# Kernel tuning notes

Measured on AMD Instinct MI355X. Metric: run time of the kernel, lower is better.

## Reference

```python
import jax, jax.numpy as jnp
import numpy as np

B, T, H = 128, 500, 512  # batch, time steps, hidden size; wx has 2H features


def setup_inputs() -> dict:
    key = jax.random.key(0)
    k1, k2, k3, k4 = jax.random.split(key, 4)
    wx = jax.random.normal(k1, (B, T, 2 * H), dtype=jnp.float32)
    u = jax.random.normal(k2, (2 * H, H), dtype=jnp.float32) * 0.05  # recurrent weight
    ht = jax.random.normal(k3, (B, H), dtype=jnp.float32)
    drop_mask = jax.random.uniform(k4, (B, H), dtype=jnp.float32)
    return {"wx": wx, "u": u, "ht": ht, "drop_mask": drop_mask}


def reference(wx, u, ht, drop_mask):
    """LiGRU cell forward: sequential recurrence over time via lax.scan.

    wx: [B, T, 2H] linearly transformed input
    u:  [2H, H]    recurrent weight
    ht: [B, H]     initial hidden state
    drop_mask: [B, H] dropout mask applied to candidate at every step
    Returns (ht, zt, at, hcand) each [B, T, H].
    """
    uT = u.T  # [H, 2H]

    def step(h, wx_t):
        gates = wx_t + h @ uT              # [B, 2H]
        at, zt_pre = jnp.split(gates, 2, axis=1)
        zt = jax.nn.sigmoid(zt_pre)
        hcand = jax.nn.relu(at) * drop_mask  # act='relu'
        h_new = h * zt + (1.0 - zt) * hcand
        return h_new, (h_new, zt, at, hcand)

    wx_t_major = jnp.swapaxes(wx, 0, 1)     # [T, B, 2H]
    _, (hs, zs, ats, hcs) = jax.lax.scan(step, ht, wx_t_major)
    tr = lambda x: jnp.swapaxes(x, 0, 1)    # [T,B,H] -> [B,T,H]
    return tr(hs), tr(zs), tr(ats), tr(hcs)
```

## Files before the change

### kernel.cpp

```cpp
#include <hip/hip_runtime.h>
#include <hip/hip_fp16.h>

#define BB 128
#define TT 500
#define HH 512
#define TWOH 1024
#define KB 16

typedef _Float16 f16x8 __attribute__((ext_vector_type(8)));
typedef float f32x4 __attribute__((ext_vector_type(4)));
typedef unsigned long long u64;

#define WS_U16_HALVES (TWOH * HH)
#define HX_WORDS (8 * 2 * 16 * HH)

__global__ void prep_kernel(const float* __restrict__ u,
                            const float* __restrict__ ht,
                            __half* __restrict__ u16,
                            unsigned* __restrict__ hx) {
  int i = blockIdx.x * blockDim.x + threadIdx.x;
  if (i < WS_U16_HALVES) u16[i] = __float2half(u[i]);
  if (i < HX_WORDS) {
    int g = i >> 14, rem = i & 16383;
    int par = rem >> 13, m = (rem >> 9) & 15, k = rem & 511;
    unsigned val;
    if (par == 0) {
      int R = g * 16 + m;
      val = (unsigned)__half_as_ushort(__float2half(ht[(size_t)R * HH + k]));
    } else {
      val = 0xFFFF0000u;
    }
    hx[i] = val;
  }
}

#define TAGMASK 0xFFFF0000FFFF0000ull

__global__ __launch_bounds__(256, 1) void ligru_mfma(
    const float* __restrict__ wx, const __half* __restrict__ u16,
    const float* __restrict__ ht, const float* __restrict__ mask,
    float* __restrict__ out, unsigned* __restrict__ hx) {
  const int tid = threadIdx.x;
  const int lane = tid & 63;
  const int w = tid >> 6;
  const int l15 = lane & 15;
  const int q = lane >> 4;
  const int b = blockIdx.x;
  const int g = b >> 3;
  const int s = b & 7;
  const int row0 = g * 16;
  const int j = s * 64 + w * 16 + l15;

  const bool own = (tid >= s * 32) && (tid < s * 32 + 32);

  __shared__ alignas(16) char hsm[2][16 * 1024];

  f16x8 bf[KB][2];
#pragma unroll
  for (int kb = 0; kb < KB; ++kb) {
    bf[kb][0] = *(const f16x8*)(u16 + (size_t)j * HH + kb * 32 + q * 8);
    bf[kb][1] = *(const f16x8*)(u16 + (size_t)(HH + j) * HH + kb * 32 + q * 8);
  }

  float hreg[4], mreg[4];
#pragma unroll
  for (int r = 0; r < 4; ++r) {
    size_t off = (size_t)(row0 + 4 * q + r) * HH + j;
    mreg[r] = mask[off];
    hreg[r] = ht[off];
  }

  const size_t BTH = (size_t)BB * TT * HH;
  float* out_h = out;
  float* out_z = out + BTH;
  float* out_a = out + 2 * BTH;
  float* out_hc = out + 3 * BTH;

  const u64* hxg = (const u64*)hx + ((size_t)g << 13);

  u64 qw[16];
#pragma unroll
  for (int pp = 0; pp < 16; ++pp)
    qw[pp] = __hip_atomic_load(hxg + pp * 256 + tid, __ATOMIC_RELAXED,
                               __HIP_MEMORY_SCOPE_AGENT);

  float wxa[4], wxz[4], wxa_n[4], wxz_n[4];
#pragma unroll
  for (int r = 0; r < 4; ++r) {
    size_t base = (size_t)(row0 + 4 * q + r) * TT * TWOH + j;
    wxa[r] = wx[base];
    wxz[r] = wx[base + HH];
  }

  for (int t = 0; t < TT; ++t) {
    const int par = t & 1;

    {
      const int tn = (t + 1 < TT) ? t + 1 : t;
#pragma unroll
      for (int r = 0; r < 4; ++r) {
        size_t base = ((size_t)(row0 + 4 * q + r) * TT + tn) * TWOH + j;
        wxa_n[r] = wx[base];
        wxz_n[r] = wx[base + HH];
      }
    }

    {
      const bool skip = own && (t > 0);
      const u64* src = hxg + par * 4096 + tid;
      const u64 tagp = ((u64)(unsigned)t << 48) | ((u64)(unsigned)t << 16);
      bool ok = true;
#pragma unroll
      for (int pp = 0; pp < 16; ++pp) ok &= ((qw[pp] & TAGMASK) == tagp);
      ok |= skip;
      if (!__all(ok)) {
        if (!skip) {
#pragma unroll
          for (int pp = 0; pp < 16; ++pp)
            qw[pp] = __hip_atomic_load(src + pp * 256, __ATOMIC_RELAXED,
                                       __HIP_MEMORY_SCOPE_AGENT);
          ok = true;
#pragma unroll
          for (int pp = 0; pp < 16; ++pp) ok &= ((qw[pp] & TAGMASK) == tagp);
        }
        int bail = 0;
        while (!__all(ok)) {
          __builtin_amdgcn_s_sleep(1);
          if (!skip) {
#pragma unroll
            for (int pp = 0; pp < 16; ++pp)
              qw[pp] = __hip_atomic_load(src + pp * 256, __ATOMIC_RELAXED,
                                         __HIP_MEMORY_SCOPE_AGENT);
            ok = true;
#pragma unroll
            for (int pp = 0; pp < 16; ++pp) ok &= ((qw[pp] & TAGMASK) == tagp);
          }
          if (++bail > (1 << 15)) break;
        }
      }
    }

    if (!(own && t > 0)) {
      char* dst = hsm[par];
#pragma unroll
      for (int pp = 0; pp < 16; ++pp) {
        unsigned d0 = (unsigned)qw[pp], d1 = (unsigned)(qw[pp] >> 32);
        unsigned pk = (d0 & 0xFFFFu) | (d1 << 16);
        *(unsigned*)(dst + ((pp * 1024 + tid * 4) ^ ((pp & 7) << 4))) = pk;
      }
    }
    __syncthreads();

    f32x4 acc0 = {0.f, 0.f, 0.f, 0.f}, acc1 = {0.f, 0.f, 0.f, 0.f};
#pragma unroll
    for (int kb = 0; kb < KB; ++kb) {
      int off = (l15 * 1024 + kb * 64 + q * 16) ^ ((l15 & 7) << 4);
      f16x8 af = *(const f16x8*)(hsm[par] + off);
      acc0 = __builtin_amdgcn_mfma_f32_16x16x32_f16(af, bf[kb][0], acc0, 0, 0, 0);
      acc1 = __builtin_amdgcn_mfma_f32_16x16x32_f16(af, bf[kb][1], acc1, 0, 0, 0);
    }

    unsigned* hd = hx + ((size_t)(g * 2 + (par ^ 1)) << 13);
    const unsigned tg = (unsigned)(t + 1) << 16;
    char* ldst = hsm[par ^ 1];
    float atv[4], ztv[4], hcv[4];
    __half hh[4];
#pragma unroll
    for (int r = 0; r < 4; ++r) {
      float at = acc0[r] + wxa[r];
      float zp = acc1[r] + wxz[r];
      float zt = 1.f / (1.f + __expf(-zp));
      float hc = fmaxf(at, 0.f) * mreg[r];
      float hn = hreg[r] * zt + (1.f - zt) * hc;
      hreg[r] = hn;
      hh[r] = __float2half(hn);
      __hip_atomic_store(hd + (4 * q + r) * HH + j,
                         tg | (unsigned)__half_as_ushort(hh[r]),
                         __ATOMIC_RELAXED, __HIP_MEMORY_SCOPE_AGENT);
      atv[r] = at;
      ztv[r] = zt;
      hcv[r] = hc;
    }

#pragma unroll
    for (int r = 0; r < 4; ++r) {
      const int m = 4 * q + r;
      *(__half*)(ldst + ((m * 1024 + j * 2) ^ ((m & 7) << 4))) = hh[r];
    }

    if (t + 1 < TT && !own) {
      const u64* srcn = hxg + (par ^ 1) * 4096 + tid;
#pragma unroll
      for (int pp = 0; pp < 16; ++pp)
        qw[pp] = __hip_atomic_load(srcn + pp * 256, __ATOMIC_RELAXED,
                                   __HIP_MEMORY_SCOPE_AGENT);
    }

#pragma unroll
    for (int r = 0; r < 4; ++r) {
      size_t oi = ((size_t)(row0 + 4 * q + r) * TT + t) * HH + j;
      __builtin_nontemporal_store(hreg[r], &out_h[oi]);
      __builtin_nontemporal_store(ztv[r], &out_z[oi]);
      __builtin_nontemporal_store(atv[r], &out_a[oi]);
      __builtin_nontemporal_store(hcv[r], &out_hc[oi]);
    }

#pragma unroll
    for (int r = 0; r < 4; ++r) {
      wxa[r] = wxa_n[r];
      wxz[r] = wxz_n[r];
    }
  }
}

extern "C" void kernel_launch(void* const* d_in, const int* in_sizes, int n_in,
                              void* d_out, int out_size, void* d_ws,
                              size_t ws_size, hipStream_t stream) {
  const float* wx = (const float*)d_in[0];
  const float* u = (const float*)d_in[1];
  const float* ht = (const float*)d_in[2];
  const float* mask = (const float*)d_in[3];
  float* out = (float*)d_out;

  __half* u16 = (__half*)d_ws;
  unsigned* hx = (unsigned*)(u16 + WS_U16_HALVES);

  hipLaunchKernelGGL(prep_kernel, dim3(2048), dim3(256), 0, stream, u, ht, u16,
                     hx);
  hipLaunchKernelGGL(ligru_mfma, dim3(64), dim3(256), 0, stream, wx, u16, ht,
                     mask, out, hx);
}
```

Before: 1.390 ms.

## Replace per-step block barrier with per-source LDS counters for incremental MFMA consumption

Each wave now polls only its own 32-lane slice of the exchanged hidden state and bumps a shared-memory counter per source slice once that slice is written to LDS. The MFMA loop waits on the counter for each k-block pair before consuming it, so work can begin on slices that have already arrived instead of waiting for all peers. The aim is to overlap waiting on slow producer blocks with computation. It adds LDS atomic spin loops and still keeps a __syncthreads at the end of each step, so any gain depends on arrival skew between producers.

```diff
diff --git a/kernel.cpp b/kernel.cpp
--- a/kernel.cpp
+++ b/kernel.cpp
@@ -50,10 +50,13 @@
   const int s = b & 7;
   const int row0 = g * 16;
   const int j = s * 64 + w * 16 + l15;
-
-  const bool own = (tid >= s * 32) && (tid < s * 32 + 32);
+  const int psrc = tid >> 5;
+  const bool own = (psrc == s);
 
   __shared__ alignas(16) char hsm[2][16 * 1024];
+  __shared__ unsigned cnt[2][8];
+
+  if (tid < 16) cnt[tid >> 3][tid & 7] = 0;
 
   f16x8 bf[KB][2];
 #pragma unroll
@@ -92,6 +95,8 @@
     wxz[r] = wx[base + HH];
   }
 
+  __syncthreads();
+
   for (int t = 0; t < TT; ++t) {
     const int par = t & 1;
 
@@ -105,55 +110,51 @@
       }
     }
 
-    {
-      const bool skip = own && (t > 0);
+    if (!(own && t > 0)) {
       const u64* src = hxg + par * 4096 + tid;
       const u64 tagp = ((u64)(unsigned)t << 48) | ((u64)(unsigned)t << 16);
       bool ok = true;
 #pragma unroll
       for (int pp = 0; pp < 16; ++pp) ok &= ((qw[pp] & TAGMASK) == tagp);
-      ok |= skip;
-      if (!__all(ok)) {
-        if (!skip) {
-#pragma unroll
-          for (int pp = 0; pp < 16; ++pp)
-            qw[pp] = __hip_atomic_load(src + pp * 256, __ATOMIC_RELAXED,
-                                       __HIP_MEMORY_SCOPE_AGENT);
-          ok = true;
-#pragma unroll
-          for (int pp = 0; pp < 16; ++pp) ok &= ((qw[pp] & TAGMASK) == tagp);
+      int bail = 0;
+      bool first = true;
+      while (!ok && bail < (1 << 15)) {
+        if (!first) __builtin_amdgcn_s_sleep(1);
+        first = false;
+#pragma unroll
+        for (int pp = 0; pp < 16; ++pp)
+          qw[pp] = __hip_atomic_load(src + pp * 256, __ATOMIC_RELAXED,
+                                     __HIP_MEMORY_SCOPE_AGENT);
+        ok = true;
+#pragma unroll
+        for (int pp = 0; pp < 16; ++pp) ok &= ((qw[pp] & TAGMASK) == tagp);
+        ++bail;
+      }
+      {
+        char* dst = hsm[par];
+#pragma unroll
+        for (int pp = 0; pp < 16; ++pp) {
+          unsigned d0 = (unsigned)qw[pp], d1 = (unsigned)(qw[pp] >> 32);
+          unsigned pk = (d0 & 0xFFFFu) | (d1 << 16);
+          *(unsigned*)(dst + ((pp * 1024 + tid * 4) ^ ((pp & 7) << 4))) = pk;
         }
-        int bail = 0;
-        while (!__all(ok)) {
-          __builtin_amdgcn_s_sleep(1);
-          if (!skip) {
-#pragma unroll
-            for (int pp = 0; pp < 16; ++pp)
-              qw[pp] = __hip_atomic_load(src + pp * 256, __ATOMIC_RELAXED,
-                                         __HIP_MEMORY_SCOPE_AGENT);
-            ok = true;
-#pragma unroll
-            for (int pp = 0; pp < 16; ++pp) ok &= ((qw[pp] & TAGMASK) == tagp);
-          }
-          if (++bail > (1 << 15)) break;
+      }
+      __hip_atomic_fetch_add(&cnt[par][psrc], 1u, __ATOMIC_RELEASE,
+                             __HIP_MEMORY_SCOPE_WORKGROUP);
+    }
+
+    f32x4 acc0 = {0.f, 0.f, 0.f, 0.f}, acc1 = {0.f, 0.f, 0.f, 0.f};
+    const unsigned target = 32u * ((unsigned)(t >> 1) + 1u);
+#pragma unroll
+    for (int kb = 0; kb < KB; ++kb) {
+      const int p = kb >> 1;
+      if (!(p == s && t > 0)) {
+        int bl = 0;
+        while (__hip_atomic_load(&cnt[par][p], __ATOMIC_ACQUIRE,
+                                 __HIP_MEMORY_SCOPE_WORKGROUP) < target &&
+               ++bl < (1 << 16)) {
         }
       }
-    }
-
-    if (!(own && t > 0)) {
-      char* dst = hsm[par];
-#pragma unroll
-      for (int pp = 0; pp < 16; ++pp) {
-        unsigned d0 = (unsigned)qw[pp], d1 = (unsigned)(qw[pp] >> 32);
-        unsigned pk = (d0 & 0xFFFFu) | (d1 << 16);
-        *(unsigned*)(dst + ((pp * 1024 + tid * 4) ^ ((pp & 7) << 4))) = pk;
-      }
-    }
-    __syncthreads();
-
-    f32x4 acc0 = {0.f, 0.f, 0.f, 0.f}, acc1 = {0.f, 0.f, 0.f, 0.f};
-#pragma unroll
-    for (int kb = 0; kb < KB; ++kb) {
       int off = (l15 * 1024 + kb * 64 + q * 16) ^ ((l15 & 7) << 4);
       f16x8 af = *(const f16x8*)(hsm[par] + off);
       acc0 = __builtin_amdgcn_mfma_f32_16x16x32_f16(af, bf[kb][0], acc0, 0, 0, 0);
@@ -210,6 +211,8 @@
       wxa[r] = wxa_n[r];
       wxz[r] = wxz_n[r];
     }
+
+    __syncthreads();
   }
 }
 
```

New measurement: 1.958 ms. 1.41x slower.
